# Performance work log

Hardware: AMD Instinct MI355X
Metric: run time of the kernel (lower is better)

## Reference

```python
import jax, jax.numpy as jnp
import numpy as np


def _lstm_layer(x_seq, w_ih, w_hh, b_ih, b_hh):
    """One LSTM layer, batch_first x_seq [B,T,D]; PyTorch gate order i,f,g,o."""
    B, T, _ = x_seq.shape
    H = w_hh.shape[1]
    # precompute input contribution for all timesteps: [B,T,4H]
    xg = jnp.einsum('btd,gd->btg', x_seq, w_ih) + b_ih + b_hh
    xg_t = jnp.swapaxes(xg, 0, 1)  # [T,B,4H]

    def step(carry, g_in):
        h, c = carry
        g = g_in + h @ w_hh.T  # [B,4H]
        i, f, gg, o = jnp.split(g, 4, axis=-1)
        i = jax.nn.sigmoid(i)
        f = jax.nn.sigmoid(f)
        gg = jnp.tanh(gg)
        o = jax.nn.sigmoid(o)
        c = f * c + i * gg
        h = o * jnp.tanh(c)
        return (h, c), h

    h0 = jnp.zeros((B, H), x_seq.dtype)
    c0 = jnp.zeros((B, H), x_seq.dtype)
    (_, _), hs = jax.lax.scan(step, (h0, c0), xg_t)
    return jnp.swapaxes(hs, 0, 1)  # [B,T,H]


def setup_inputs() -> dict:
    key = jax.random.key(0)
    ks = jax.random.split(key, 12)
    V, E, H, B, T = 50000, 100, 64, 256, 512
    s = 0.1
    emb = jax.random.normal(ks[0], (V, E), jnp.float32) * s
    emb = emb.at[0].set(0.0)  # padding_idx=0
    return {
        'x': jax.random.randint(ks[1], (B, T), 0, V),
        'emb': emb,
        'w_ih0': jax.random.normal(ks[2], (4 * H, E), jnp.float32) * s,
        'w_hh0': jax.random.normal(ks[3], (4 * H, H), jnp.float32) * s,
        'b_ih0': jax.random.normal(ks[4], (4 * H,), jnp.float32) * s,
        'b_hh0': jax.random.normal(ks[5], (4 * H,), jnp.float32) * s,
        'w_ih1': jax.random.normal(ks[6], (4 * H, H), jnp.float32) * s,
        'w_hh1': jax.random.normal(ks[7], (4 * H, H), jnp.float32) * s,
        'b_ih1': jax.random.normal(ks[8], (4 * H,), jnp.float32) * s,
        'b_hh1': jax.random.normal(ks[9], (4 * H,), jnp.float32) * s,
        'fc_w': jax.random.normal(ks[10], (1, H), jnp.float32) * s,
        'fc_b': jax.random.normal(ks[11], (1,), jnp.float32) * s,
    }


def reference(x, emb, w_ih0, w_hh0, b_ih0, b_hh0,
              w_ih1, w_hh1, b_ih1, b_hh1, fc_w, fc_b):
    emb_eff = emb.at[0].set(0.0)  # padding_idx=0 row stays zero
    embedded = emb_eff[x]  # [B,T,E]
    h1 = _lstm_layer(embedded, w_ih0, w_hh0, b_ih0, b_hh0)
    h2 = _lstm_layer(h1, w_ih1, w_hh1, b_ih1, b_hh1)
    last = h2[:, -1, :]  # [B,H]
    # eval mode: dropout is identity
    act = jax.nn.relu(last)
    out = act @ fc_w.T + fc_b  # [B,1]
    return jax.nn.sigmoid(out)
```

## Files before the change

### kernel.cpp

```cpp
#include <hip/hip_runtime.h>

#define VSZ 50000
#define ESZ 100
#define HSZ 64
#define GSZ 256
#define BSZ 256
#define TSZ 512

__device__ __forceinline__ float fast_rcp(float x) { return __builtin_amdgcn_rcpf(x); }
__device__ __forceinline__ float sigmoid_f(float x) { return fast_rcp(1.f + __expf(-x)); }
__device__ __forceinline__ float tanh_f(float x) {
    float e = __expf(2.f * x);
    return 1.f - 2.f * fast_rcp(e + 1.f);
}

__global__ __launch_bounds__(256) void build_table(
    const float* __restrict__ emb, const float* __restrict__ w_ih0,
    const float* __restrict__ b_ih0, const float* __restrict__ b_hh0,
    float* __restrict__ Gt)
{
    const int g = threadIdx.x;
    const int row0 = blockIdx.x * 32;
    const int col = ((g & 63) << 2) + (g >> 6);

    float w[ESZ];
    #pragma unroll
    for (int e = 0; e < ESZ; e += 4) {
        float4 v = *(const float4*)(w_ih0 + g * ESZ + e);
        w[e] = v.x; w[e + 1] = v.y; w[e + 2] = v.z; w[e + 3] = v.w;
    }
    const float bias = b_ih0[g] + b_hh0[g];

    #pragma unroll 1
    for (int r = row0; r < row0 + 32 && r < VSZ; r += 4) {
        const int off0 = __builtin_amdgcn_readfirstlane(r * ESZ);
        const float* e0 = emb + off0;
        const float* e1 = e0 + ESZ;
        const float* e2 = e0 + 2 * ESZ;
        const float* e3 = e0 + 3 * ESZ;
        float a0 = bias, a1 = 0.f, a2 = 0.f, a3 = 0.f;
        float b0 = bias, b1 = 0.f, b2 = 0.f, b3 = 0.f;
        float c0 = bias, c1 = 0.f, c2 = 0.f, c3 = 0.f;
        float d0 = bias, d1 = 0.f, d2 = 0.f, d3 = 0.f;
        #pragma unroll
        for (int e = 0; e < ESZ; e += 4) {
            a0 += e0[e    ] * w[e    ]; a1 += e0[e + 1] * w[e + 1];
            a2 += e0[e + 2] * w[e + 2]; a3 += e0[e + 3] * w[e + 3];
            b0 += e1[e    ] * w[e    ]; b1 += e1[e + 1] * w[e + 1];
            b2 += e1[e + 2] * w[e + 2]; b3 += e1[e + 3] * w[e + 3];
            c0 += e2[e    ] * w[e    ]; c1 += e2[e + 1] * w[e + 1];
            c2 += e2[e + 2] * w[e + 2]; c3 += e2[e + 3] * w[e + 3];
            d0 += e3[e    ] * w[e    ]; d1 += e3[e + 1] * w[e + 1];
            d2 += e3[e + 2] * w[e + 2]; d3 += e3[e + 3] * w[e + 3];
        }
        Gt[(size_t)r       * GSZ + col] = (a0 + a1) + (a2 + a3);
        Gt[(size_t)(r + 1) * GSZ + col] = (b0 + b1) + (b2 + b3);
        Gt[(size_t)(r + 2) * GSZ + col] = (c0 + c1) + (c2 + c3);
        Gt[(size_t)(r + 3) * GSZ + col] = (d0 + d1) + (d2 + d3);
    }
}

__device__ __forceinline__ void sync_lds() {
    asm volatile("s_waitcnt lgkmcnt(0)\n\ts_barrier" ::: "memory");
}

#define LD4(ptr, off) (*(const float4*)((ptr) + (off)))
#define PIN4(v) asm volatile("" : "+v"(v.x), "+v"(v.y), "+v"(v.z), "+v"(v.w))
#define DOT4(acc, Sa, Sb, Sc, Sd)                                  \
    acc += Sa.x*H0.x; acc += Sa.y*H0.y; acc += Sa.z*H0.z; acc += Sa.w*H0.w; \
    acc += Sb.x*H1.x; acc += Sb.y*H1.y; acc += Sb.z*H1.z; acc += Sb.w*H1.w; \
    acc += Sc.x*H2.x; acc += Sc.y*H2.y; acc += Sc.z*H2.z; acc += Sc.w*H2.w; \
    acc += Sd.x*H3.x; acc += Sd.y*H3.y; acc += Sd.z*H3.z; acc += Sd.w*H3.w

__global__ __launch_bounds__(768, 2) void lstm_fused(
    const int* __restrict__ x, const float* __restrict__ Gt,
    const float* __restrict__ w_hh0,
    const float* __restrict__ w_ih1, const float* __restrict__ w_hh1,
    const float* __restrict__ b_ih1, const float* __restrict__ b_hh1,
    const float* __restrict__ fc_w, const float* __restrict__ fc_b,
    float* __restrict__ out)
{
    const int tid = threadIdx.x;
    const int b   = blockIdx.x;
    const bool isA = tid < 256;
    const int lt  = isA ? tid : (tid - 256);
    const int q   = isA ? (lt >> 2) : (lt >> 3);
    const int j   = isA ? (lt & 3) : (lt & 7);
    const int gt  = j & 3;

    __shared__ __align__(16) float h0b[2][HSZ];
    __shared__ __align__(16) float h1b[2][HSZ];
    __shared__ int xtok[TSZ];

    const float* pw1 = isA ? (w_hh0 + q * HSZ + 16 * j)
                           : (w_ih1 + q * HSZ + 8 * j);
    const float* pw2 = isA ? (w_hh0 + q * HSZ + 16 * j + 8)
                           : (w_hh1 + q * HSZ + 8 * j);

    float4 S00=LD4(pw1,0),     S01=LD4(pw1,4),     S02=LD4(pw2,0),     S03=LD4(pw2,4);
    float4 S10=LD4(pw1,4096),  S11=LD4(pw1,4100),  S12=LD4(pw2,4096),  S13=LD4(pw2,4100);
    float4 S20=LD4(pw1,8192),  S21=LD4(pw1,8196),  S22=LD4(pw2,8192),  S23=LD4(pw2,8196);
    float4 S30=LD4(pw1,12288), S31=LD4(pw1,12292), S32=LD4(pw2,12288), S33=LD4(pw2,12292);
    PIN4(S00); PIN4(S01); PIN4(S02); PIN4(S03);
    PIN4(S10); PIN4(S11); PIN4(S12); PIN4(S13);
    PIN4(S20); PIN4(S21); PIN4(S22); PIN4(S23);
    PIN4(S30); PIN4(S31); PIN4(S32); PIN4(S33);

    float addend_b = 0.f;
    if (!isA) addend_b = b_ih1[gt * HSZ + q] + b_hh1[gt * HSZ + q];
    const float mco = (gt == 2) ?  2.f : -1.f;
    const float Aco = (gt == 2) ?  1.f :  0.f;
    const float Bco = (gt == 2) ? -2.f :  1.f;

    if (tid < 128)      ((float*)h0b)[tid] = 0.f;
    else if (tid < 256) ((float*)h1b)[tid - 128] = 0.f;
    if (tid < TSZ) xtok[tid] = x[b * TSZ + tid];
    __syncthreads();

    float c = 0.f;
    float xg_cur = 0.f;
    if (isA) xg_cur = Gt[(size_t)xtok[0] * GSZ + 4 * q + j];

    #pragma unroll 1
    for (int k = 0; k <= TSZ; ++k) {
        float xg_nxt = 0.f;
        if (isA && k + 1 < TSZ)
            xg_nxt = Gt[(size_t)xtok[k + 1] * GSZ + 4 * q + j];

        const float4* h0v = (const float4*)h0b[(k ^ 1) & 1];
        const float4* h1v = (const float4*)h1b[k & 1];
        const float4* hA  = h0v + (isA ? 4 * j : 2 * j);
        const float4* hB  = isA ? (h0v + 4 * j + 2) : (h1v + 2 * j);
        float4 H0 = hA[0], H1 = hA[1], H2 = hB[0], H3 = hB[1];

        float d0 = 0.f, d1 = 0.f, d2 = 0.f, d3 = 0.f;
        DOT4(d0, S00, S01, S02, S03);
        DOT4(d1, S10, S11, S12, S13);
        DOT4(d2, S20, S21, S22, S23);
        DOT4(d3, S30, S31, S32, S33);

        if (!isA) {
            d0 += __shfl_xor(d0, 4, 64); d1 += __shfl_xor(d1, 4, 64);
            d2 += __shfl_xor(d2, 4, 64); d3 += __shfl_xor(d3, 4, 64);
        }
        const bool lo2 = (j & 2) == 0;
        float u  = lo2 ? d2 : d0, v = lo2 ? d3 : d1;
        float ru = __shfl_xor(u, 2, 64), rv = __shfl_xor(v, 2, 64);
        float aa = (lo2 ? d0 : d2) + ru;
        float bb = (lo2 ? d1 : d3) + rv;
        const bool lo1 = (j & 1) == 0;
        float ws = lo1 ? bb : aa;
        float rw = __shfl_xor(ws, 1, 64);
        float s  = (lo1 ? aa : bb) + rw;

        s += isA ? xg_cur : addend_b;
        float e   = __expf(mco * s);
        float act = fmaf(Bco, fast_rcp(1.f + e), Aco);

        float o1 = __shfl_xor(act, 1, 64);
        float ge = lo1 ? act : o1;
        float go = lo1 ? o1 : act;
        float pe = __shfl_xor(ge, 2, 64), po = __shfl_xor(go, 2, 64);
        float iact = lo2 ? ge : pe;
        float fact = lo2 ? go : po;
        float gact = lo2 ? pe : ge;
        float oact = lo2 ? po : go;

        const bool active = isA ? (k < TSZ) : (k >= 1);
        if (active) {
            c = fact * c + iact * gact;
            float hn = oact * tanh_f(c);
            if (j == 0) {
                if (isA) h0b[k & 1][q] = hn;
                else     h1b[(k ^ 1) & 1][q] = hn;
            }
        }
        xg_cur = xg_nxt;
        sync_lds();
    }

    if (tid < HSZ) {
        float v = fmaxf(h1b[1][tid], 0.f) * fc_w[tid];
        #pragma unroll
        for (int off = 32; off > 0; off >>= 1) v += __shfl_down(v, off, 64);
        if (tid == 0) out[b] = sigmoid_f(v + fc_b[0]);
    }
}

extern "C" void kernel_launch(void* const* d_in, const int* in_sizes, int n_in,
                              void* d_out, int out_size, void* d_ws, size_t ws_size,
                              hipStream_t stream) {
    const int*   x     = (const int*)  d_in[0];
    const float* emb   = (const float*)d_in[1];
    const float* w_ih0 = (const float*)d_in[2];
    const float* w_hh0 = (const float*)d_in[3];
    const float* b_ih0 = (const float*)d_in[4];
    const float* b_hh0 = (const float*)d_in[5];
    const float* w_ih1 = (const float*)d_in[6];
    const float* w_hh1 = (const float*)d_in[7];
    const float* b_ih1 = (const float*)d_in[8];
    const float* b_hh1 = (const float*)d_in[9];
    const float* fc_w  = (const float*)d_in[10];
    const float* fc_b  = (const float*)d_in[11];
    float* out = (float*)d_out;

    float* Gt = (float*)d_ws;

    build_table<<<dim3((VSZ + 31) / 32), dim3(256), 0, stream>>>(
        emb, w_ih0, b_ih0, b_hh0, Gt);
    lstm_fused<<<dim3(BSZ), dim3(768), 0, stream>>>(
        x, Gt, w_hh0, w_ih1, w_hh1, b_ih1, b_hh1, fc_w, fc_b, out);
}
```

Baseline: 538.1 us.

## Use fp16 packed dot products and remap LSTM threads to 1024 per block

```diff
diff --git a/kernel.cpp b/kernel.cpp
--- a/kernel.cpp
+++ b/kernel.cpp
@@ -7,11 +7,20 @@
 #define BSZ 256
 #define TSZ 512
 
+typedef _Float16 halfv2 __attribute__((ext_vector_type(2)));
+typedef _Float16 half8  __attribute__((ext_vector_type(8)));
+
 __device__ __forceinline__ float fast_rcp(float x) { return __builtin_amdgcn_rcpf(x); }
 __device__ __forceinline__ float sigmoid_f(float x) { return fast_rcp(1.f + __expf(-x)); }
 __device__ __forceinline__ float tanh_f(float x) {
     float e = __expf(2.f * x);
     return 1.f - 2.f * fast_rcp(e + 1.f);
+}
+__device__ __forceinline__ float fdot2f(halfv2 a, halfv2 b, float c) {
+    return __builtin_amdgcn_fdot2(a, b, c, false);
+}
+__device__ __forceinline__ halfv2 h2at(half8 v, int m) {
+    halfv2 r; r[0] = v[2 * m]; r[1] = v[2 * m + 1]; return r;
 }
 
 __global__ __launch_bounds__(256) void build_table(
@@ -63,16 +72,9 @@
 __device__ __forceinline__ void sync_lds() {
     asm volatile("s_waitcnt lgkmcnt(0)\n\ts_barrier" ::: "memory");
 }
-
-#define LD4(ptr, off) (*(const float4*)((ptr) + (off)))
-#define PIN4(v) asm volatile("" : "+v"(v.x), "+v"(v.y), "+v"(v.z), "+v"(v.w))
-#define DOT4(acc, Sa, Sb, Sc, Sd)                                  \
-    acc += Sa.x*H0.x; acc += Sa.y*H0.y; acc += Sa.z*H0.z; acc += Sa.w*H0.w; \
-    acc += Sb.x*H1.x; acc += Sb.y*H1.y; acc += Sb.z*H1.z; acc += Sb.w*H1.w; \
-    acc += Sc.x*H2.x; acc += Sc.y*H2.y; acc += Sc.z*H2.z; acc += Sc.w*H2.w; \
-    acc += Sd.x*H3.x; acc += Sd.y*H3.y; acc += Sd.z*H3.z; acc += Sd.w*H3.w
-
-__global__ __launch_bounds__(768, 2) void lstm_fused(
+#define PINH(v) asm volatile("" : "+v"(v))
+
+__global__ void lstm_fused(
     const int* __restrict__ x, const float* __restrict__ Gt,
     const float* __restrict__ w_hh0,
     const float* __restrict__ w_ih1, const float* __restrict__ w_hh1,
@@ -80,99 +82,111 @@
     const float* __restrict__ fc_w, const float* __restrict__ fc_b,
     float* __restrict__ out)
 {
-    const int tid = threadIdx.x;
-    const int b   = blockIdx.x;
-    const bool isA = tid < 256;
-    const int lt  = isA ? tid : (tid - 256);
-    const int q   = isA ? (lt >> 2) : (lt >> 3);
-    const int j   = isA ? (lt & 3) : (lt & 7);
-    const int gt  = j & 3;
-
-    __shared__ __align__(16) float h0b[2][HSZ];
-    __shared__ __align__(16) float h1b[2][HSZ];
+    const int tid  = threadIdx.x;
+    const int b    = blockIdx.x;
+    const int lane = tid & 63;
+    const int wv   = tid >> 6;
+    const int q    = wv * 4 + (lane >> 4);
+    const int gt   = (lane >> 2) & 3;
+    const int j    = lane & 3;
+    const int grow = gt * HSZ + q;
+
+    __shared__ __align__(16) _Float16 h0b[2][HSZ];
+    __shared__ __align__(16) _Float16 h1b[2][HSZ];
     __shared__ int xtok[TSZ];
 
-    const float* pw1 = isA ? (w_hh0 + q * HSZ + 16 * j)
-                           : (w_ih1 + q * HSZ + 8 * j);
-    const float* pw2 = isA ? (w_hh0 + q * HSZ + 16 * j + 8)
-                           : (w_hh1 + q * HSZ + 8 * j);
-
-    float4 S00=LD4(pw1,0),     S01=LD4(pw1,4),     S02=LD4(pw2,0),     S03=LD4(pw2,4);
-    float4 S10=LD4(pw1,4096),  S11=LD4(pw1,4100),  S12=LD4(pw2,4096),  S13=LD4(pw2,4100);
-    float4 S20=LD4(pw1,8192),  S21=LD4(pw1,8196),  S22=LD4(pw2,8192),  S23=LD4(pw2,8196);
-    float4 S30=LD4(pw1,12288), S31=LD4(pw1,12292), S32=LD4(pw2,12288), S33=LD4(pw2,12292);
-    PIN4(S00); PIN4(S01); PIN4(S02); PIN4(S03);
-    PIN4(S10); PIN4(S11); PIN4(S12); PIN4(S13);
-    PIN4(S20); PIN4(S21); PIN4(S22); PIN4(S23);
-    PIN4(S30); PIN4(S31); PIN4(S32); PIN4(S33);
-
-    float addend_b = 0.f;
-    if (!isA) addend_b = b_ih1[gt * HSZ + q] + b_hh1[gt * HSZ + q];
+    halfv2 w0[8], wi[8], wh[8];
+    {
+        const float* p0 = w_hh0 + grow * HSZ + 16 * j;
+        const float* pi = w_ih1 + grow * HSZ + 16 * j;
+        const float* ph = w_hh1 + grow * HSZ + 16 * j;
+        #pragma unroll
+        for (int m = 0; m < 4; ++m) {
+            float4 f = *(const float4*)(p0 + 4 * m);
+            w0[2*m]   = halfv2{(_Float16)f.x, (_Float16)f.y};
+            w0[2*m+1] = halfv2{(_Float16)f.z, (_Float16)f.w};
+            f = *(const float4*)(pi + 4 * m);
+            wi[2*m]   = halfv2{(_Float16)f.x, (_Float16)f.y};
+            wi[2*m+1] = halfv2{(_Float16)f.z, (_Float16)f.w};
+            f = *(const float4*)(ph + 4 * m);
+            wh[2*m]   = halfv2{(_Float16)f.x, (_Float16)f.y};
+            wh[2*m+1] = halfv2{(_Float16)f.z, (_Float16)f.w};
+        }
+    }
+    #pragma unroll
+    for (int m = 0; m < 8; ++m) { PINH(w0[m]); PINH(wi[m]); PINH(wh[m]); }
+
+    const float bias1 = b_ih1[grow] + b_hh1[grow];
     const float mco = (gt == 2) ?  2.f : -1.f;
     const float Aco = (gt == 2) ?  1.f :  0.f;
     const float Bco = (gt == 2) ? -2.f :  1.f;
 
-    if (tid < 128)      ((float*)h0b)[tid] = 0.f;
-    else if (tid < 256) ((float*)h1b)[tid - 128] = 0.f;
+    if (tid < 128)      ((_Float16*)h0b)[tid] = (_Float16)0.f;
+    else if (tid < 256) ((_Float16*)h1b)[tid - 128] = (_Float16)0.f;
     if (tid < TSZ) xtok[tid] = x[b * TSZ + tid];
     __syncthreads();
 
-    float c = 0.f;
+    float c0 = 0.f, c1 = 0.f;
     float xg_cur = 0.f;
-    if (isA) xg_cur = Gt[(size_t)xtok[0] * GSZ + 4 * q + j];
+    if (j == 0) xg_cur = Gt[(size_t)xtok[0] * GSZ + 4 * q + gt];
 
     #pragma unroll 1
     for (int k = 0; k <= TSZ; ++k) {
         float xg_nxt = 0.f;
-        if (isA && k + 1 < TSZ)
-            xg_nxt = Gt[(size_t)xtok[k + 1] * GSZ + 4 * q + j];
-
-        const float4* h0v = (const float4*)h0b[(k ^ 1) & 1];
-        const float4* h1v = (const float4*)h1b[k & 1];
-        const float4* hA  = h0v + (isA ? 4 * j : 2 * j);
-        const float4* hB  = isA ? (h0v + 4 * j + 2) : (h1v + 2 * j);
-        float4 H0 = hA[0], H1 = hA[1], H2 = hB[0], H3 = hB[1];
-
-        float d0 = 0.f, d1 = 0.f, d2 = 0.f, d3 = 0.f;
-        DOT4(d0, S00, S01, S02, S03);
-        DOT4(d1, S10, S11, S12, S13);
-        DOT4(d2, S20, S21, S22, S23);
-        DOT4(d3, S30, S31, S32, S33);
-
-        if (!isA) {
-            d0 += __shfl_xor(d0, 4, 64); d1 += __shfl_xor(d1, 4, 64);
-            d2 += __shfl_xor(d2, 4, 64); d3 += __shfl_xor(d3, 4, 64);
-        }
-        const bool lo2 = (j & 2) == 0;
-        float u  = lo2 ? d2 : d0, v = lo2 ? d3 : d1;
-        float ru = __shfl_xor(u, 2, 64), rv = __shfl_xor(v, 2, 64);
-        float aa = (lo2 ? d0 : d2) + ru;
-        float bb = (lo2 ? d1 : d3) + rv;
-        const bool lo1 = (j & 1) == 0;
-        float ws = lo1 ? bb : aa;
-        float rw = __shfl_xor(ws, 1, 64);
-        float s  = (lo1 ? aa : bb) + rw;
-
-        s += isA ? xg_cur : addend_b;
-        float e   = __expf(mco * s);
-        float act = fmaf(Bco, fast_rcp(1.f + e), Aco);
-
-        float o1 = __shfl_xor(act, 1, 64);
-        float ge = lo1 ? act : o1;
-        float go = lo1 ? o1 : act;
-        float pe = __shfl_xor(ge, 2, 64), po = __shfl_xor(go, 2, 64);
-        float iact = lo2 ? ge : pe;
-        float fact = lo2 ? go : po;
-        float gact = lo2 ? pe : ge;
-        float oact = lo2 ? po : go;
-
-        const bool active = isA ? (k < TSZ) : (k >= 1);
-        if (active) {
-            c = fact * c + iact * gact;
-            float hn = oact * tanh_f(c);
-            if (j == 0) {
-                if (isA) h0b[k & 1][q] = hn;
-                else     h1b[(k ^ 1) & 1][q] = hn;
+        if (j == 0 && k + 1 < TSZ)
+            xg_nxt = Gt[(size_t)xtok[k + 1] * GSZ + 4 * q + gt];
+
+        const _Float16* h0p = h0b[(k ^ 1) & 1];
+        const _Float16* h1p = h1b[k & 1];
+        half8 ha0 = *(const half8*)(h0p + 16 * j);
+        half8 ha1 = *(const half8*)(h0p + 16 * j + 8);
+        float d = 0.f, e = 0.f;
+        #pragma unroll
+        for (int m = 0; m < 4; ++m) {
+            halfv2 h = h2at(ha0, m);
+            d = fdot2f(w0[m], h, d); e = fdot2f(wi[m], h, e);
+        }
+        #pragma unroll
+        for (int m = 0; m < 4; ++m) {
+            halfv2 h = h2at(ha1, m);
+            d = fdot2f(w0[4+m], h, d); e = fdot2f(wi[4+m], h, e);
+        }
+        half8 hb0 = *(const half8*)(h1p + 16 * j);
+        half8 hb1 = *(const half8*)(h1p + 16 * j + 8);
+        #pragma unroll
+        for (int m = 0; m < 4; ++m) {
+            e = fdot2f(wh[m],   h2at(hb0, m), e);
+            e = fdot2f(wh[4+m], h2at(hb1, m), e);
+        }
+
+        d += __shfl_xor(d, 1, 64); d += __shfl_xor(d, 2, 64);
+        e += __shfl_xor(e, 1, 64); e += __shfl_xor(e, 2, 64);
+
+        float aL0 = 0.f, aL1 = 0.f;
+        if (j == 0) {
+            float s0 = d + xg_cur;
+            aL0 = fmaf(Bco, fast_rcp(1.f + __expf(mco * s0)), Aco);
+            float s1 = e + bias1;
+            aL1 = fmaf(Bco, fast_rcp(1.f + __expf(mco * s1)), Aco);
+        }
+
+        float f0 = __shfl_xor(aL0, 4, 64);
+        float g0 = __shfl_xor(aL0, 8, 64);
+        float o0 = __shfl_xor(aL0, 12, 64);
+        float f1 = __shfl_xor(aL1, 4, 64);
+        float g1 = __shfl_xor(aL1, 8, 64);
+        float o1 = __shfl_xor(aL1, 12, 64);
+
+        if ((lane & 15) == 0) {
+            if (k < TSZ) {
+                c0 = f0 * c0 + aL0 * g0;
+                float hn = o0 * tanh_f(c0);
+                h0b[k & 1][q] = (_Float16)hn;
+            }
+            if (k >= 1) {
+                c1 = f1 * c1 + aL1 * g1;
+                float hn = o1 * tanh_f(c1);
+                h1b[(k ^ 1) & 1][q] = (_Float16)hn;
             }
         }
         xg_cur = xg_nxt;
@@ -180,7 +194,7 @@
     }
 
     if (tid < HSZ) {
-        float v = fmaxf(h1b[1][tid], 0.f) * fc_w[tid];
+        float v = fmaxf((float)h1b[1][tid], 0.f) * fc_w[tid];
         #pragma unroll
         for (int off = 32; off > 0; off >>= 1) v += __shfl_down(v, off, 64);
         if (tid == 0) out[b] = sigmoid_f(v + fc_b[0]);
@@ -208,6 +222,6 @@
 
     build_table<<<dim3((VSZ + 31) / 32), dim3(256), 0, stream>>>(
         emb, w_ih0, b_ih0, b_hh0, Gt);
-    lstm_fused<<<dim3(BSZ), dim3(768), 0, stream>>>(
+    lstm_fused<<<dim3(BSZ), dim3(1024), 0, stream>>>(
         x, Gt, w_hh0, w_ih1, w_hh1, b_ih1, b_hh1, fc_w, fc_b, out);
 }
```

After: 607.6 us. 12.9% more time.
